# Kernel optimization log

Measured on AMD Instinct MI355X. Metric: run time of the kernel, lower is better.

## Reference

```python
import jax, jax.numpy as jnp
import numpy as np

PI = float(np.pi)


def _make_grid(H, W, stride, k, delta):
    """Gnomonic (tangent-plane) sampling grid for one spherical conv layer.
    Returns rows (Ho, K) and cols (Ho, Wo, K) of fractional pixel coords."""
    Ho, Wo = H // stride, W // stride
    j = jnp.arange(k, dtype=jnp.float32) - (k - 1) / 2.0
    t = jnp.tan(delta / k * j)                      # tangent-plane tap coords
    yy = jnp.repeat(t, k)                           # (K,) vertical
    xx = jnp.tile(t, k)                             # (K,) horizontal
    rho = jnp.sqrt(xx ** 2 + yy ** 2)
    rho_s = jnp.where(rho == 0, 1.0, rho)
    nu = jnp.arctan(rho)
    # latitude of each output row center (equirect: row -> colatitude)
    lat0 = PI / 2 - (jnp.arange(Ho, dtype=jnp.float32) * stride + 0.5) * (PI / H)
    sl, cl = jnp.sin(lat0)[:, None], jnp.cos(lat0)[:, None]   # (Ho,1)
    sn, cn = jnp.sin(nu)[None, :], jnp.cos(nu)[None, :]       # (1,K)
    lat = jnp.arcsin(jnp.clip(cn * sl + (yy[None, :] / rho_s[None, :]) * sn * cl, -1.0, 1.0))
    dlon = jnp.arctan2(xx[None, :] * sn, rho[None, :] * cl * cn - yy[None, :] * sl * sn)
    rows = (PI / 2 - lat) / PI * H - 0.5            # (Ho,K) fractional row
    dcol = dlon / (2 * PI) * W                      # (Ho,K) longitude offset in px
    cols = (jnp.arange(Wo, dtype=jnp.float32) * stride)[None, :, None] + dcol[:, None, :]
    return rows, cols


def _bilinear(x, rows, cols):
    """x: (B,C,H,W); rows (Ho,K); cols (Ho,Wo,K). Latitude clamped, longitude wrapped.
    Returns patches (B,C,Ho,Wo,K)."""
    B, C, H, W = x.shape
    r0 = jnp.floor(rows); wr = (rows - r0)[:, None, :]
    c0 = jnp.floor(cols); wc = cols - c0
    r0i = jnp.clip(r0, 0, H - 1).astype(jnp.int32)
    r1i = jnp.clip(r0 + 1, 0, H - 1).astype(jnp.int32)
    c0i = jnp.mod(c0.astype(jnp.int32), W)
    c1i = jnp.mod(c0i + 1, W)

    def g(ri, ci):
        return x[:, :, ri[:, None, :], ci]          # (B,C,Ho,Wo,K)

    return (g(r0i, c0i) * (1 - wr) * (1 - wc) + g(r0i, c1i) * (1 - wr) * wc
            + g(r1i, c0i) * wr * (1 - wc) + g(r1i, c1i) * wr * wc)


def _sconv(x, w, b, delta, stride):
    k = int(round(np.sqrt(w.shape[-1])))
    rows, cols = _make_grid(x.shape[2], x.shape[3], stride, k, delta)
    p = _bilinear(x, rows, cols)                    # (B,C,Ho,Wo,K)
    return jnp.einsum('bchwk,ock->bohw', p, w) + b[None, :, None, None]


def _bn_relu(x, g, b):
    m = x.mean((0, 2, 3), keepdims=True)
    v = jnp.mean((x - m) ** 2, (0, 2, 3), keepdims=True)  # biased var (torch BN train)
    return jax.nn.relu((x - m) / jnp.sqrt(v + 1e-5) * g[None, :, None, None] + b[None, :, None, None])


def _up2(x):
    return jnp.repeat(jnp.repeat(x, 2, axis=2), 2, axis=3)


def _forward(input, w1, b1, g1, bb1, w2, b2, g2, bb2, w3, b3, g3, bb3,
             w31, b31, g31, bb31, w4, b4, g4, bb4, w41, b41, g41, bb41,
             w5, b5, g5, bb5, w6, b6, g6, bb6):
    x1 = _bn_relu(_sconv(input, w1, b1, PI / 32, 2), g1, bb1)
    x2 = _bn_relu(_sconv(x1, w2, b2, PI / 16, 2), g2, bb2)
    x3 = _bn_relu(_sconv(x2, w3, b3, PI / 4, 2), g3, bb3)
    x31 = _bn_relu(_sconv(x3, w31, b31, PI / 4, 1), g31, bb31)
    x4 = _bn_relu(_sconv(x31, w4, b4, PI / 2, 2), g4, bb4)
    x41 = _bn_relu(_sconv(x4, w41, b41, PI / 2, 1), g41, bb41)
    x5 = _bn_relu(_sconv(jnp.concatenate([_up2(x41), x31], 1), w5, b5, PI / 4, 1), g5, bb5)
    x6 = _bn_relu(_sconv(jnp.concatenate([_up2(x5), x2], 1), w6, b6, PI / 8, 1), g6, bb6)
    return x6


_CFGS = [('1', 32, 6, 7), ('2', 64, 32, 5), ('3', 128, 64, 5), ('31', 128, 128, 3),
         ('4', 256, 128, 3), ('41', 256, 256, 3), ('5', 256, 384, 3), ('6', 128, 320, 3)]


def setup_inputs() -> dict:
    key = jax.random.key(0)
    inp = {'input': jax.random.normal(jax.random.fold_in(key, 0), (4, 6, 256, 512), jnp.float32)}
    for i, (s, o, c, kk) in enumerate(_CFGS):
        kw = jax.random.fold_in(key, i + 1)
        inp['w' + s] = jax.random.normal(kw, (o, c, kk * kk), jnp.float32) / np.float32(np.sqrt(c * kk * kk))
        inp['b' + s] = jnp.zeros((o,), jnp.float32)
        inp['g' + s] = jnp.ones((o,), jnp.float32)
        inp['bb' + s] = jnp.zeros((o,), jnp.float32)
    return inp


def reference(input, w1, b1, g1, bb1, w2, b2, g2, bb2, w3, b3, g3, bb3,
              w31, b31, g31, bb31, w4, b4, g4, bb4, w41, b41, g41, bb41,
              w5, b5, g5, bb5, w6, b6, g6, bb6):
    return _forward(input, w1, b1, g1, bb1, w2, b2, g2, bb2, w3, b3, g3, bb3,
                    w31, b31, g31, bb31, w4, b4, g4, bb4, w41, b41, g41, bb41,
                    w5, b5, g5, bb5, w6, b6, g6, bb6)
```

## Files before the change

### kernel.cpp

```cpp
#include <hip/hip_runtime.h>
#include <cstddef>
#include <cstdint>

#define PI_F 3.14159265358979323846f

typedef __attribute__((ext_vector_type(8))) short short8;
typedef __attribute__((ext_vector_type(4))) float floatx4;

template<int V> struct IC { static constexpr int value = V; };

__device__ __forceinline__ short f2bf(float f) {
    union { float f; unsigned u; } v; v.f = f;
    unsigned r = v.u + 0x7FFFu + ((v.u >> 16) & 1u);
    return (short)(r >> 16);
}

__global__ __launch_bounds__(256) void wtrans_kernel(
    const float* __restrict__ A, short* __restrict__ Abf,
    int M, int Mpad, int K2, int C, int Cp, int Kp, int Korig)
{
    int idx = blockIdx.x * 256 + threadIdx.x;
    if (idx >= Mpad * Kp) return;
    int m = idx / Kp;
    int k = idx - m * Kp;
    int tap = (unsigned)k / (unsigned)Cp;
    int c   = k - tap * Cp;
    float v = 0.f;
    if (m < M && tap < K2 && c < C) v = A[(size_t)m * Korig + c * K2 + tap];
    Abf[idx] = f2bf(v);
}

__global__ __launch_bounds__(256) void zero_kernel(float* __restrict__ p, int n)
{
    int i = blockIdx.x * 256 + threadIdx.x;
    if (i < n) p[i] = 0.f;
}

__global__ __launch_bounds__(256) void zero3_kernel(
    float* __restrict__ a, int na, float* __restrict__ b, int nb,
    float* __restrict__ c, int nc)
{
    int i = blockIdx.x * 256 + threadIdx.x;
    if (i < na) { a[i] = 0.f; return; }
    i -= na;
    if (i < nb) { b[i] = 0.f; return; }
    i -= nb;
    if (i < nc) c[i] = 0.f;
}

#define BNT 64
#define BKT 32
#define LDK 40

template<int MW, int SK, int LGW, int UP, int LGWO, int CS>
__global__ __launch_bounds__(256) void sconv_mfma_kernel(
    const short* __restrict__ Abf,
    const float* __restrict__ src1, const float* __restrict__ src2,
    float2* __restrict__ part, int nBlkN,
    int C1, int Ctot, int Cp, int H, int W, int up1,
    int K2, int ksz, int stride, int lWo, int lHo, float delta,
    float* __restrict__ Y, int M, int Kp, int N, int lgM)
{
    __shared__ short Bs[(LGW != 0) ? 1 : 2][BNT][LDK];
    __shared__ float4 tab[64];
    extern __shared__ __align__(16) char dynLds[];

    constexpr int LGSK = (SK == 1) ? 0 : ((SK == 2) ? 1 : 2);

    const int tid = threadIdx.x;
    const int total = gridDim.x;
    const int pid = blockIdx.x;
    const int logical = (pid & 7) * (total >> 3) + (pid >> 3);
    const int mblk = logical & ((1 << lgM) - 1);
    const int rest = logical >> lgM;
    const int kslice = rest & (SK - 1);
    const int nblk = rest >> LGSK;
    const int m0 = mblk * (MW * 64);
    const int n0 = nblk * BNT;

    const int Wo  = 1 << lWo;
    const int Ho  = 1 << lHo;
    const int HW  = 1 << (lWo + lHo);

    const int nHo  = (lWo >= 6) ? 1 : (BNT >> lWo);
    const int nEnt = nHo * K2;
    const int hoBase = (n0 >> lWo) & (Ho - 1);
    if (tid < nEnt) {
        int hoL = tid / K2;
        int i   = tid - hoL * K2;
        int ho_g = hoBase + hoL;
        int jy = i / ksz, jx = i - jy * ksz;
        float halfk = (ksz - 1) * 0.5f;
        float yy = tanf(delta / (float)ksz * ((float)jy - halfk));
        float xx = tanf(delta / (float)ksz * ((float)jx - halfk));
        float rho = sqrtf(xx * xx + yy * yy);
        float rho_s = (rho == 0.f) ? 1.f : rho;
        float nu = atanf(rho);
        float lat0 = PI_F * 0.5f - ((float)(ho_g * stride) + 0.5f) * (PI_F / (float)H);
        float sl = sinf(lat0), cl = cosf(lat0);
        float sn = sinf(nu),  cn = cosf(nu);
        float arg = cn * sl + (yy / rho_s) * sn * cl;
        arg = fminf(1.f, fmaxf(-1.f, arg));
        float lat = asinf(arg);
        float dlon = atan2f(xx * sn, rho * cl * cn - yy * sl * sn);
        float row = (PI_F * 0.5f - lat) / PI_F * (float)H - 0.5f;
        float dcol = dlon / (2.f * PI_F) * (float)W;
        float r0f = floorf(row);
        float fr = row - r0f;
        int r0 = (int)r0f;
        int r0i = min(max(r0, 0), H - 1);
        int r1i = min(max(r0 + 1, 0), H - 1);
        tab[tid] = make_float4(fr, dcol, __int_as_float(r0i), __int_as_float(r1i));
    }

    const int nn    = tid & 63;
    const int kslot = tid >> 6;
    const int n_s  = n0 + nn;
    const int wo_s = n_s & (Wo - 1);
    const int hoL_s = nn >> lWo;
    const int b_s  = n_s >> (lWo + lHo);
    const int tabBase = hoL_s * K2;
    const float wo_px = (float)(wo_s * stride);
    const int Hs = H >> up1, Ws = W >> up1;
    const int plane1 = Hs * Ws;
    const int plane2 = H * W;
    const unsigned boff1 = (unsigned)__builtin_amdgcn_readfirstlane(
        (int)(b_s * C1 * plane1));
    const unsigned boff2 = (unsigned)__builtin_amdgcn_readfirstlane(
        (int)(b_s * (Ctot - C1) * plane2));

    const int Tper = (Kp / BKT) / SK;
    const int t0 = kslice * Tper;
    const bool smallC = (Cp < 32);
    int tap, cb;
    if (smallC) { tap = kslot; cb = 0; }
    else {
        int prog = t0 * BKT;
        tap = prog / Cp;
        cb  = prog - tap * Cp + kslot * 8;
    }
    const int dtap = smallC ? (32 / Cp) : 0;

    const int wave = tid >> 6;
    const int wrow = wave * (MW * 16);
    const int lane = tid & 63;
    const int l16  = lane & 15;
    const int quad = lane >> 4;

    const short* pA[MW];
#pragma unroll
    for (int i = 0; i < MW; i++)
        pA[i] = Abf + (size_t)(m0 + wrow + i * 16 + l16) * Kp + quad * 8;

    floatx4 acc[MW][4];
#pragma unroll
    for (int i = 0; i < MW; i++)
#pragma unroll
        for (int j = 0; j < 4; j++)
            acc[i][j] = (floatx4){0.f, 0.f, 0.f, 0.f};

    if constexpr (LGW == 0) {
        __syncthreads();

        for (int t = t0; t < t0 + Tper; t++) {
            const int k0 = t * BKT;
            const int buf = t & 1;
            const int tapS = __builtin_amdgcn_readfirstlane(tap);
            const int cbS  = __builtin_amdgcn_readfirstlane(cb);
            {
                const int tapc = min(tapS, K2 - 1);
                const float4 e = tab[tabBase + tapc];
                const float fr = e.x;
                const float col = wo_px + e.y;
                const int r0i = __float_as_int(e.z);
                const int r1i = __float_as_int(e.w);
                const float cf = floorf(col);
                const float fc = col - cf;
                const int c0 = ((int)cf) & (W - 1);
                const int c1 = (c0 + 1) & (W - 1);
                const float w11 = fr * fc;
                const float w10 = fr - w11;
                const float w01 = fc - w11;
                const float w00 = 1.f - fr - fc + w11;

                const char* sbase; unsigned o00, o01, o10, o11, planeB;
                if (cbS < C1) {
                    const int ra = (r0i >> up1) * Ws, rb = (r1i >> up1) * Ws;
                    const int ca = c0 >> up1, cx = c1 >> up1;
                    const unsigned base = boff1 + (unsigned)cbS * (unsigned)plane1;
                    o00 = (base + ra + ca) * 4u; o01 = (base + ra + cx) * 4u;
                    o10 = (base + rb + ca) * 4u; o11 = (base + rb + cx) * 4u;
                    planeB = (unsigned)plane1 * 4u; sbase = (const char*)src1;
                } else {
                    const int ra = r0i * W, rb = r1i * W;
                    const unsigned base = boff2 + (unsigned)(cbS - C1) * (unsigned)plane2;
                    o00 = (base + ra + c0) * 4u; o01 = (base + ra + c1) * 4u;
                    o10 = (base + rb + c0) * 4u; o11 = (base + rb + c1) * 4u;
                    planeB = (unsigned)plane2 * 4u; sbase = (const char*)src2;
                }

                if constexpr (CS > 0) {
                    float q00[CS], q01[CS], q10[CS], q11[CS];
#pragma unroll
                    for (int j = 0; j < CS; j++) {
                        q00[j] = *(const float*)(sbase + o00);
                        q01[j] = *(const float*)(sbase + o01);
                        q10[j] = *(const float*)(sbase + o10);
                        q11[j] = *(const float*)(sbase + o11);
                        o00 += planeB; o01 += planeB; o10 += planeB; o11 += planeB;
                    }
                    unsigned pk[4];
#pragma unroll
                    for (int jj = 0; jj < 4; jj++) {
                        if (2 * jj < CS) {
                            float v0 = w00 * q00[2 * jj] + w01 * q01[2 * jj]
                                     + w10 * q10[2 * jj] + w11 * q11[2 * jj];
                            float v1 = 0.f;
                            if (2 * jj + 1 < CS)
                                v1 = w00 * q00[2 * jj + 1] + w01 * q01[2 * jj + 1]
                                   + w10 * q10[2 * jj + 1] + w11 * q11[2 * jj + 1];
                            unsigned rr;
                            asm("v_cvt_pk_bf16_f32 %0, %1, %2"
                                : "=v"(rr) : "v"(v0), "v"(v1));
                            pk[jj] = rr;
                        } else {
                            pk[jj] = 0u;
                        }
                    }
                    *(uint4*)&Bs[buf][nn][kslot * 8] =
                        make_uint4(pk[0], pk[1], pk[2], pk[3]);
                } else {
                    float q00[8], q01[8], q10[8], q11[8];
#pragma unroll
                    for (int j = 0; j < 8; j++) {
                        q00[j] = *(const float*)(sbase + o00);
                        q01[j] = *(const float*)(sbase + o01);
                        q10[j] = *(const float*)(sbase + o10);
                        q11[j] = *(const float*)(sbase + o11);
                        o00 += planeB; o01 += planeB; o10 += planeB; o11 += planeB;
                    }
                    unsigned pk[4];
#pragma unroll
                    for (int jj = 0; jj < 4; jj++) {
                        float v0 = w00 * q00[2 * jj]     + w01 * q01[2 * jj]
                                 + w10 * q10[2 * jj]     + w11 * q11[2 * jj];
                        float v1 = w00 * q00[2 * jj + 1] + w01 * q01[2 * jj + 1]
                                 + w10 * q10[2 * jj + 1] + w11 * q11[2 * jj + 1];
                        unsigned r;
                        asm("v_cvt_pk_bf16_f32 %0, %1, %2"
                            : "=v"(r) : "v"(v0), "v"(v1));
                        pk[jj] = r;
                    }
                    *(uint4*)&Bs[buf][nn][kslot * 8] =
                        make_uint4(pk[0], pk[1], pk[2], pk[3]);
                }
            }
            __syncthreads();

            short8 af[MW];
#pragma unroll
            for (int i = 0; i < MW; i++)
                af[i] = *(const short8*)(pA[i] + k0);
            short8 bfv[4];
#pragma unroll
            for (int j = 0; j < 4; j++)
                bfv[j] = *(const short8*)&Bs[buf][j * 16 + l16][quad * 8];
#pragma unroll
            for (int i = 0; i < MW; i++)
#pragma unroll
                for (int j = 0; j < 4; j++)
                    acc[i][j] = __builtin_amdgcn_mfma_f32_16x16x32_bf16(
                        af[i], bfv[j], acc[i][j], 0, 0, 0);

            if (smallC) { tap += dtap; }
            else { cb += 32; if (cb >= Cp) { cb -= Cp; tap++; } }
        }
    } else {
        constexpr int WC    = 1 << LGW;
        constexpr int LGWS1 = LGW - UP;
        constexpr int NHO   = (LGWO >= 6) ? 1 : (64 >> LGWO);
        constexpr int NHO2  = NHO * 2;
        constexpr int LG2NHO = (NHO == 4) ? 3 : ((NHO == 2) ? 2 : 1);
        constexpr int NU    = 64 * NHO;
        const int kslotU = __builtin_amdgcn_readfirstlane(kslot);

        auto stageTile = [&](int tapT, int cbT) {
            const bool s1 = (cbT < C1);
            const float* srcT = s1 ? src1 : src2;
            const int lgWt = s1 ? LGWS1 : LGW;
            const int upT  = s1 ? UP : 0;
            const int plT  = s1 ? plane1 : plane2;
            const unsigned chB = s1
                ? (boff1 + (unsigned)cbT * (unsigned)plane1)
                : (boff2 + (unsigned)(cbT - C1) * (unsigned)plane2);
            const int tapc2 = min(tapT, K2 - 1);
            const int lgLPU = lgWt - 2;
            const int NIw = (NU << lgWt) >> 10;
            const int uW  = lane >> lgLPU;
            const unsigned colB = (unsigned)(lane & ((1 << lgLPU) - 1)) << 2;
            for (int ii = 0; ii < NIw; ii++) {
                const int idx = kslotU * NIw + ii;
                const int u = (idx << (6 - lgLPU)) + uW;
                const int chL = u >> LG2NHO;
                const int rem = u & (NHO2 - 1);
                const int hoL = rem & (NHO - 1);
                const float4 e = tab[hoL * K2 + tapc2];
                const float rsel = (rem >> (LG2NHO - 1)) ? e.w : e.z;
                const int r = __float_as_int(rsel) >> upT;
                const float* gp = srcT + (chB + (unsigned)chL * (unsigned)plT
                                          + ((unsigned)r << lgWt) + colB);
                __builtin_amdgcn_global_load_lds(
                    (const __attribute__((address_space(1))) void*)gp,
                    (__attribute__((address_space(3))) void*)(dynLds + (size_t)idx * 1024),
                    16, 0, 0);
            }
        };

        int tapS, cb0S;
        {
            int prog = t0 * BKT;
            tapS = prog / Cp;
            cb0S = prog - tapS * Cp;
        }

        __syncthreads();

        stageTile(tapS, cb0S);
        short8 afc[MW];
#pragma unroll
        for (int i2 = 0; i2 < MW; i2++)
            afc[i2] = *(const short8*)(pA[i2] + t0 * BKT);

        for (int t = t0; t < t0 + Tper; t++) {
            tapS = __builtin_amdgcn_readfirstlane(tapS);
            cb0S = __builtin_amdgcn_readfirstlane(cb0S);
            const bool isS1 = (cb0S < C1);
            const int tapcI  = min(tapS, K2 - 1);

            asm volatile("s_waitcnt vmcnt(0)" ::: "memory");
            __syncthreads();

            auto interpStore = [&](auto lgwc, auto upc) {
                constexpr int LGWSRC = decltype(lgwc)::value;
                constexpr int UPX    = decltype(upc)::value;
                constexpr int STEPR  = NHO << LGWSRC;
                constexpr int STEPC  = NHO2 << LGWSRC;
                const float4 e2 = tab[tabBase + tapcI];
                const float fr = e2.x;
                const float col = wo_px + e2.y;
                const float cf = floorf(col);
                const float fc = col - cf;
                const int c0 = ((int)cf) & (WC - 1);
                const int c1 = (c0 + 1) & (WC - 1);
                const int c0s = c0 >> UPX, c1s = c1 >> UPX;
                const float w11 = fr * fc;
                const float w10 = fr - w11;
                const float w01 = fc - w11;
                const float w00 = 1.f - fr - fc + w11;
                const float* rowsF = (const float*)dynLds;
                const float* pc0 = rowsF
                    + ((((kslot * 8) << LG2NHO) + hoL_s) << LGWSRC) + c0s;
                const float* pc1 = pc0 + (c1s - c0s);
                float vv[8];
#pragma unroll
                for (int j = 0; j < 8; j++) {
                    const float x00 = pc0[0];
                    const float x10 = pc0[STEPR];
                    const float x01 = pc1[0];
                    const float x11 = pc1[STEPR];
                    vv[j] = w00 * x00 + w01 * x01 + w10 * x10 + w11 * x11;
                    pc0 += STEPC; pc1 += STEPC;
                }
                unsigned pk[4];
#pragma unroll
                for (int jj = 0; jj < 4; jj++) {
                    unsigned rr;
                    asm("v_cvt_pk_bf16_f32 %0, %1, %2"
                        : "=v"(rr) : "v"(vv[2 * jj]), "v"(vv[2 * jj + 1]));
                    pk[jj] = rr;
                }
                *(uint4*)&Bs[0][nn][kslot * 8] =
                    make_uint4(pk[0], pk[1], pk[2], pk[3]);
            };
            if (isS1) interpStore(IC<LGWS1>{}, IC<UP>{});
            else      interpStore(IC<LGW>{},   IC<0>{});

            __syncthreads();

            int tapN = tapS, cbN = cb0S + BKT;
            if (cbN >= Cp) { cbN = 0; tapN = tapS + 1; }
            const bool more = (t + 1 < t0 + Tper);
            short8 afn[MW];
            if (more) {
#pragma unroll
                for (int i2 = 0; i2 < MW; i2++)
                    afn[i2] = *(const short8*)(pA[i2] + (t + 1) * BKT);
                stageTile(tapN, cbN);
            }

            short8 bfr[4];
#pragma unroll
            for (int j = 0; j < 4; j++)
                bfr[j] = *(const short8*)&Bs[0][j * 16 + l16][quad * 8];
#pragma unroll
            for (int i2 = 0; i2 < MW; i2++)
#pragma unroll
                for (int j = 0; j < 4; j++)
                    acc[i2][j] = __builtin_amdgcn_mfma_f32_16x16x32_bf16(
                        afc[i2], bfr[j], acc[i2][j], 0, 0, 0);

            tapS = tapN; cb0S = cbN;
            if (more) {
#pragma unroll
                for (int i2 = 0; i2 < MW; i2++) afc[i2] = afn[i2];
            }
        }
    }

    if (SK == 1) {
#pragma unroll
        for (int i = 0; i < MW; i++) {
#pragma unroll
            for (int rr = 0; rr < 4; rr++) {
                const int m = m0 + wrow + i * 16 + quad * 4 + rr;
                const bool mv = (m < M);
                float s = 0.f, q = 0.f;
#pragma unroll
                for (int j = 0; j < 4; j++) {
                    const int n = n0 + j * 16 + l16;
                    const float v = acc[i][j][rr];
                    s += v; q += v * v;
                    if (mv) {
                        const int wo = n & (Wo - 1);
                        const int r  = n >> lWo;
                        const int ho = r & (Ho - 1);
                        const int b_ = r >> lHo;
                        Y[((size_t)b_ * M + m) * HW + (ho << lWo) + wo] = v;
                    }
                }
#pragma unroll
                for (int mask = 1; mask < 16; mask <<= 1) {
                    s += __shfl_xor(s, mask);
                    q += __shfl_xor(q, mask);
                }
                if (mv && l16 == 0)
                    part[(size_t)m * nBlkN + nblk] = make_float2(s, q);
            }
        }
    } else {
#pragma unroll
        for (int i = 0; i < MW; i++) {
#pragma unroll
            for (int j = 0; j < 4; j++) {
                const int n = n0 + j * 16 + l16;
                const int wo = n & (Wo - 1);
                const int r  = n >> lWo;
                const int ho = r & (Ho - 1);
                const int b_ = r >> lHo;
#pragma unroll
                for (int rr = 0; rr < 4; rr++) {
                    const int m = m0 + wrow + i * 16 + quad * 4 + rr;
                    if (m < M)
                        unsafeAtomicAdd(
                            &Y[((size_t)b_ * M + m) * HW + (ho << lWo) + wo],
                            acc[i][j][rr]);
                }
            }
        }
    }
}

__global__ __launch_bounds__(256) void bn_stats8_kernel(
    const float* __restrict__ Y, float2* __restrict__ part,
    int Co, int HW, int B)
{
    int co = blockIdx.x;
    int sp = blockIdx.y;
    int tid = threadIdx.x;
    int Nt = B * HW;
    int len = Nt >> 3;
    int start = sp * len, end = start + len;
    float s = 0.f, q = 0.f;
    for (int idx = start + tid; idx < end; idx += 256) {
        int b = idx / HW; int o = idx - b * HW;
        float v = Y[((size_t)b * Co + co) * HW + o];
        s += v; q += v * v;
    }
    __shared__ float sh_s[256], sh_q[256];
    sh_s[tid] = s; sh_q[tid] = q;
    __syncthreads();
    for (int off = 128; off > 0; off >>= 1) {
        if (tid < off) { sh_s[tid] += sh_s[tid + off]; sh_q[tid] += sh_q[tid + off]; }
        __syncthreads();
    }
    if (tid == 0)
        part[co * 8 + sp] = make_float2(sh_s[0], sh_q[0]);
}

__global__ __launch_bounds__(256) void bn_finalize_kernel(
    const float2* __restrict__ part, float2* __restrict__ scSf,
    const float* __restrict__ g, const float* __restrict__ bb,
    int nBlkN, int Nt)
{
    int c = blockIdx.x;
    int tid = threadIdx.x;
    double s = 0.0, q = 0.0;
    for (int k = tid; k < nBlkN; k += 256) {
        float2 p = part[(size_t)c * nBlkN + k];
        s += p.x; q += p.y;
    }
    __shared__ double sh_s[256], sh_q[256];
    sh_s[tid] = s; sh_q[tid] = q;
    __syncthreads();
    for (int off = 128; off > 0; off >>= 1) {
        if (tid < off) { sh_s[tid] += sh_s[tid + off]; sh_q[tid] += sh_q[tid + off]; }
        __syncthreads();
    }
    if (tid == 0) {
        double mean = sh_s[0] / Nt;
        double var = sh_q[0] / Nt - mean * mean;
        if (var < 0.0) var = 0.0;
        float sc = g[c] / sqrtf((float)var + 1e-5f);
        scSf[c] = make_float2(sc, bb[c] - (float)mean * sc);
    }
}

__global__ __launch_bounds__(256) void bn_apply_kernel(
    float* __restrict__ Y, const float2* __restrict__ scSf,
    int Co, int HW, int total)
{
    int idx = blockIdx.x * 256 + threadIdx.x;
    if (idx >= total) return;
    int c = (idx / HW) % Co;
    float2 s = scSf[c];
    float v = Y[idx] * s.x + s.y;
    Y[idx] = v > 0.f ? v : 0.f;
}

__global__ __launch_bounds__(256) void bn_apply_sk_kernel(
    float* __restrict__ Y, const float2* __restrict__ part,
    const float* __restrict__ g, const float* __restrict__ bb,
    int Co, int HW, int Nt, int total)
{
    int idx = blockIdx.x * 256 + threadIdx.x;
    int c = (idx / HW) % Co;
    __shared__ float s_sc, s_sf;
    if (threadIdx.x == 0) {
        double s = 0.0, q = 0.0;
        for (int p = 0; p < 8; p++) {
            float2 pp = part[c * 8 + p];
            s += pp.x; q += pp.y;
        }
        double mean = s / Nt;
        double var = q / Nt - mean * mean;
        if (var < 0.0) var = 0.0;
        float sc = g[c] / sqrtf((float)var + 1e-5f);
        s_sc = sc;
        s_sf = bb[c] - (float)mean * sc;
    }
    __syncthreads();
    if (idx >= total) return;
    float v = Y[idx] * s_sc + s_sf;
    Y[idx] = v > 0.f ? v : 0.f;
}

extern "C" void kernel_launch(void* const* d_in, const int* in_sizes, int n_in,
                              void* d_out, int out_size, void* d_ws, size_t ws_size,
                              hipStream_t stream)
{
    const int B = 4;
    char* ws = (char*)d_ws;
    size_t off = 0;
    auto allocb = [&](size_t bytes) -> void* {
        void* p = ws + off;
        off = (off + bytes + 255) & ~(size_t)255;
        return p;
    };

    float2* part = (float2*)allocb((size_t)65536 * sizeof(float2));
    float2* scSf = (float2*)allocb(256 * sizeof(float2));
    float* x2  = (float*)allocb((size_t)B * 64  * 64 * 128 * 4);
    float* x31 = (float*)allocb((size_t)B * 128 * 32 * 64 * 4);
    float* Q   = (float*)allocb((size_t)B * 32  * 128 * 256 * 4);
    float* x1  = Q;
    float* x3  = Q;
    float* x4  = Q;
    float* x41 = Q + (size_t)B * 256 * 16 * 32;
    float* x5  = Q + 2 * (size_t)B * 256 * 16 * 32;

    static const int kH[8]  = {256, 128,  64,  32,  32,  16,  32,  64};
    static const int kW[8]  = {512, 256, 128,  64,  64,  32,  64, 128};
    static const int kK[8]  = {  7,   5,   5,   3,   3,   3,   3,   3};
    static const int kSt[8] = {  2,   2,   2,   1,   2,   1,   1,   1};
    static const int kC[8]  = {  6,  32,  64, 128, 128, 256, 384, 320};
    static const int kM[8]  = { 32,  64, 128, 128, 256, 256, 256, 128};
    static const int kMW[8] = {  1,   1,   1,   1,   1,   1,   2,   2};
    static const int kSK[8] = {  1,   2,   4,   4,   4,   4,   4,   2};

    int Cp_[8], Kp_[8], Mpad_[8];
    short* Abf[8];
    for (int i = 0; i < 8; i++) {
        int K2 = kK[i] * kK[i];
        int Cp = (kC[i] < 8) ? 8 : kC[i];
        int gran = 32 * kSK[i];
        int Kp = (K2 * Cp + gran - 1) / gran * gran;
        int Mpad = (kM[i] + 63) & ~63;
        Cp_[i] = Cp; Kp_[i] = Kp; Mpad_[i] = Mpad;
        Abf[i] = (short*)allocb((size_t)Mpad * Kp * sizeof(short));
    }
    (void)ws_size; (void)in_sizes; (void)n_in; (void)out_size;

    struct LCfg { const float *s1, *s2; int C1, up; float delta; int widx; float* Y; };
    const float* input = (const float*)d_in[0];
    LCfg L[8] = {
        { input, nullptr,   6, 0, PI_F / 32.f,  1, x1  },
        { x1,    nullptr,  32, 0, PI_F / 16.f,  5, x2  },
        { x2,    nullptr,  64, 0, PI_F / 4.f,   9, x3  },
        { x3,    nullptr, 128, 0, PI_F / 4.f,  13, x31 },
        { x31,   nullptr, 128, 0, PI_F / 2.f,  17, x4  },
        { x4,    nullptr, 256, 0, PI_F / 2.f,  21, x41 },
        { x41,   x31,     256, 1, PI_F / 4.f,  25, x5  },
        { x5,    x2,      256, 1, PI_F / 8.f,  29, (float*)d_out },
    };

    {
        int n_x2 = B * 64 * 64 * 128;
        int n_x31 = B * 128 * 32 * 64;
        int n_out = B * 128 * 64 * 128;
        int tot = n_x2 + n_x31 + n_out;
        zero3_kernel<<<dim3((tot + 255) / 256), dim3(256), 0, stream>>>(
            x2, n_x2, x31, n_x31, (float*)d_out, n_out);
    }

    for (int i = 0; i < 8; i++) {
        const LCfg& c = L[i];
        int H = kH[i], W = kW[i], k = kK[i], st = kSt[i];
        int Ho = H / st, Wo = W / st;
        int K2 = k * k;
        int C  = kC[i], M = kM[i];
        int HW = Ho * Wo;
        int N  = B * HW;
        int lWo = __builtin_ctz(Wo), lHo = __builtin_ctz(Ho);
        const float* Wt   = (const float*)d_in[c.widx];
        const float* gam  = (const float*)d_in[c.widx + 2];
        const float* bet  = (const float*)d_in[c.widx + 3];
        int total = B * M * HW;

        int tn = Mpad_[i] * Kp_[i];
        wtrans_kernel<<<dim3((tn + 255) / 256), dim3(256), 0, stream>>>(
            Wt, Abf[i], M, Mpad_[i], K2, C, Cp_[i], Kp_[i], C * K2);

        int MWi = kMW[i], SKi = kSK[i];
        int nBlkM = Mpad_[i] / (64 * MWi);
        int nBlkN = N / BNT;
        int totalBlk = nBlkN * nBlkM * SKi;
        int lgM = __builtin_ctz(nBlkM);

        size_t dynB = 0;
        if (i >= 2) {
            int nHo_i = (Wo >= 64) ? 1 : (64 / Wo);
            int w1 = W >> c.up;
            int wmax = c.s2 ? W : w1;
            if (w1 > wmax) wmax = w1;
            dynB = (size_t)(64 * nHo_i) * (size_t)wmax * 4u;
        }

        if (SKi > 1 && i >= 2 && i <= 6 && c.Y != x31)
            zero_kernel<<<dim3((total + 255) / 256), dim3(256), 0, stream>>>(
                c.Y, total);

        #define CONV_ARGS Abf[i], c.s1, c.s2, part, nBlkN, \
            c.C1, C, Cp_[i], H, W, c.up, K2, k, st, lWo, lHo, c.delta, \
            c.Y, M, Kp_[i], N, lgM
        #define LAUNCH(MW_, SK_, LGW_, UP_, LGWO_, CS_, DYN_) \
            sconv_mfma_kernel<MW_,SK_,LGW_,UP_,LGWO_,CS_> \
                <<<dim3(totalBlk), dim3(256), DYN_, stream>>>(CONV_ARGS)
        switch (i) {
            case 0: LAUNCH(1, 1, 0, 0, 0, 6, 0);    break;
            case 1: LAUNCH(1, 2, 0, 0, 0, 0, 0);    break;
            case 2: LAUNCH(1, 4, 7, 0, 6, 0, dynB); break;
            case 3: LAUNCH(1, 4, 6, 0, 6, 0, dynB); break;
            case 4: LAUNCH(1, 4, 6, 0, 5, 0, dynB); break;
            case 5: LAUNCH(1, 4, 5, 0, 5, 0, dynB); break;
            case 6: LAUNCH(2, 4, 6, 1, 6, 0, dynB); break;
            case 7: LAUNCH(2, 2, 7, 1, 7, 0, dynB); break;
        }
        #undef LAUNCH
        #undef CONV_ARGS

        if (SKi > 1) {
            bn_stats8_kernel<<<dim3(M, 8), dim3(256), 0, stream>>>(
                c.Y, part, M, HW, B);
            bn_apply_sk_kernel<<<dim3(total / 256), dim3(256), 0, stream>>>(
                c.Y, part, gam, bet, M, HW, N, total);
        } else {
            bn_finalize_kernel<<<dim3(M), dim3(256), 0, stream>>>(
                part, scSf, gam, bet, nBlkN, N);
            bn_apply_kernel<<<dim3(total / 256), dim3(256), 0, stream>>>(
                c.Y, scSf, M, HW, total);
        }
    }
}
```

Before: 694.7 us.

## Software-pipeline bilinear gather loads one K-step ahead in LGW==0 path

Restructures the LGW==0 main loop so the four-corner global gathers for the next K tile are issued before interpolating, storing and running MFMAs on the current tile, using two ping-pong register sets. This aims to hide gather latency behind the bf16 conversion, LDS store and MFMA work. The cost is extra VGPRs for a second set of gathered values, which may lower occupancy. Issuing one step ahead also makes the last iteration read one extra tap, which the existing min clamp on tap keeps in bounds.

```diff
diff --git a/kernel.cpp b/kernel.cpp
--- a/kernel.cpp
+++ b/kernel.cpp
@@ -160,103 +160,85 @@
             acc[i][j] = (floatx4){0.f, 0.f, 0.f, 0.f};
 
     if constexpr (LGW == 0) {
-        __syncthreads();
-
-        for (int t = t0; t < t0 + Tper; t++) {
+        constexpr int CSX = (CS > 0) ? CS : 8;
+        struct QS {
+            float q00[CSX], q01[CSX], q10[CSX], q11[CSX];
+            float w00, w01, w10, w11;
+        };
+        QS qa, qb;
+
+        auto issueQ = [&](QS& q) {
+            const int tapS = __builtin_amdgcn_readfirstlane(tap);
+            const int cbS  = __builtin_amdgcn_readfirstlane(cb);
+            const int tapc = min(tapS, K2 - 1);
+            const float4 e = tab[tabBase + tapc];
+            const float fr = e.x;
+            const float col = wo_px + e.y;
+            const int r0i = __float_as_int(e.z);
+            const int r1i = __float_as_int(e.w);
+            const float cf = floorf(col);
+            const float fc = col - cf;
+            const int c0 = ((int)cf) & (W - 1);
+            const int c1 = (c0 + 1) & (W - 1);
+            const float w11 = fr * fc;
+            q.w11 = w11;
+            q.w10 = fr - w11;
+            q.w01 = fc - w11;
+            q.w00 = 1.f - fr - fc + w11;
+
+            const char* sbase; unsigned o00, o01, o10, o11, planeB;
+            if (cbS < C1) {
+                const int ra = (r0i >> up1) * Ws, rb = (r1i >> up1) * Ws;
+                const int ca = c0 >> up1, cx = c1 >> up1;
+                const unsigned base = boff1 + (unsigned)cbS * (unsigned)plane1;
+                o00 = (base + ra + ca) * 4u; o01 = (base + ra + cx) * 4u;
+                o10 = (base + rb + ca) * 4u; o11 = (base + rb + cx) * 4u;
+                planeB = (unsigned)plane1 * 4u; sbase = (const char*)src1;
+            } else {
+                const int ra = r0i * W, rb = r1i * W;
+                const unsigned base = boff2 + (unsigned)(cbS - C1) * (unsigned)plane2;
+                o00 = (base + ra + c0) * 4u; o01 = (base + ra + c1) * 4u;
+                o10 = (base + rb + c0) * 4u; o11 = (base + rb + c1) * 4u;
+                planeB = (unsigned)plane2 * 4u; sbase = (const char*)src2;
+            }
+#pragma unroll
+            for (int j = 0; j < CSX; j++) {
+                q.q00[j] = *(const float*)(sbase + o00);
+                q.q01[j] = *(const float*)(sbase + o01);
+                q.q10[j] = *(const float*)(sbase + o10);
+                q.q11[j] = *(const float*)(sbase + o11);
+                o00 += planeB; o01 += planeB; o10 += planeB; o11 += planeB;
+            }
+            if (smallC) { tap += dtap; }
+            else { cb += 32; if (cb >= Cp) { cb -= Cp; tap++; } }
+        };
+
+        auto interpStoreD = [&](const QS& q, int buf) {
+            unsigned pk[4];
+#pragma unroll
+            for (int jj = 0; jj < 4; jj++) {
+                if (2 * jj < CSX) {
+                    float v0 = q.w00 * q.q00[2 * jj] + q.w01 * q.q01[2 * jj]
+                             + q.w10 * q.q10[2 * jj] + q.w11 * q.q11[2 * jj];
+                    float v1 = 0.f;
+                    if (2 * jj + 1 < CSX)
+                        v1 = q.w00 * q.q00[2 * jj + 1] + q.w01 * q.q01[2 * jj + 1]
+                           + q.w10 * q.q10[2 * jj + 1] + q.w11 * q.q11[2 * jj + 1];
+                    unsigned rr;
+                    asm("v_cvt_pk_bf16_f32 %0, %1, %2"
+                        : "=v"(rr) : "v"(v0), "v"(v1));
+                    pk[jj] = rr;
+                } else {
+                    pk[jj] = 0u;
+                }
+            }
+            *(uint4*)&Bs[buf][nn][kslot * 8] =
+                make_uint4(pk[0], pk[1], pk[2], pk[3]);
+        };
+
+        auto mfmaStep = [&](int t) {
             const int k0 = t * BKT;
             const int buf = t & 1;
-            const int tapS = __builtin_amdgcn_readfirstlane(tap);
-            const int cbS  = __builtin_amdgcn_readfirstlane(cb);
-            {
-                const int tapc = min(tapS, K2 - 1);
-                const float4 e = tab[tabBase + tapc];
-                const float fr = e.x;
-                const float col = wo_px + e.y;
-                const int r0i = __float_as_int(e.z);
-                const int r1i = __float_as_int(e.w);
-                const float cf = floorf(col);
-                const float fc = col - cf;
-                const int c0 = ((int)cf) & (W - 1);
-                const int c1 = (c0 + 1) & (W - 1);
-                const float w11 = fr * fc;
-                const float w10 = fr - w11;
-                const float w01 = fc - w11;
-                const float w00 = 1.f - fr - fc + w11;
-
-                const char* sbase; unsigned o00, o01, o10, o11, planeB;
-                if (cbS < C1) {
-                    const int ra = (r0i >> up1) * Ws, rb = (r1i >> up1) * Ws;
-                    const int ca = c0 >> up1, cx = c1 >> up1;
-                    const unsigned base = boff1 + (unsigned)cbS * (unsigned)plane1;
-                    o00 = (base + ra + ca) * 4u; o01 = (base + ra + cx) * 4u;
-                    o10 = (base + rb + ca) * 4u; o11 = (base + rb + cx) * 4u;
-                    planeB = (unsigned)plane1 * 4u; sbase = (const char*)src1;
-                } else {
-                    const int ra = r0i * W, rb = r1i * W;
-                    const unsigned base = boff2 + (unsigned)(cbS - C1) * (unsigned)plane2;
-                    o00 = (base + ra + c0) * 4u; o01 = (base + ra + c1) * 4u;
-                    o10 = (base + rb + c0) * 4u; o11 = (base + rb + c1) * 4u;
-                    planeB = (unsigned)plane2 * 4u; sbase = (const char*)src2;
-                }
-
-                if constexpr (CS > 0) {
-                    float q00[CS], q01[CS], q10[CS], q11[CS];
-#pragma unroll
-                    for (int j = 0; j < CS; j++) {
-                        q00[j] = *(const float*)(sbase + o00);
-                        q01[j] = *(const float*)(sbase + o01);
-                        q10[j] = *(const float*)(sbase + o10);
-                        q11[j] = *(const float*)(sbase + o11);
-                        o00 += planeB; o01 += planeB; o10 += planeB; o11 += planeB;
-                    }
-                    unsigned pk[4];
-#pragma unroll
-                    for (int jj = 0; jj < 4; jj++) {
-                        if (2 * jj < CS) {
-                            float v0 = w00 * q00[2 * jj] + w01 * q01[2 * jj]
-                                     + w10 * q10[2 * jj] + w11 * q11[2 * jj];
-                            float v1 = 0.f;
-                            if (2 * jj + 1 < CS)
-                                v1 = w00 * q00[2 * jj + 1] + w01 * q01[2 * jj + 1]
-                                   + w10 * q10[2 * jj + 1] + w11 * q11[2 * jj + 1];
-                            unsigned rr;
-                            asm("v_cvt_pk_bf16_f32 %0, %1, %2"
-                                : "=v"(rr) : "v"(v0), "v"(v1));
-                            pk[jj] = rr;
-                        } else {
-                            pk[jj] = 0u;
-                        }
-                    }
-                    *(uint4*)&Bs[buf][nn][kslot * 8] =
-                        make_uint4(pk[0], pk[1], pk[2], pk[3]);
-                } else {
-                    float q00[8], q01[8], q10[8], q11[8];
-#pragma unroll
-                    for (int j = 0; j < 8; j++) {
-                        q00[j] = *(const float*)(sbase + o00);
-                        q01[j] = *(const float*)(sbase + o01);
-                        q10[j] = *(const float*)(sbase + o10);
-                        q11[j] = *(const float*)(sbase + o11);
-                        o00 += planeB; o01 += planeB; o10 += planeB; o11 += planeB;
-                    }
-                    unsigned pk[4];
-#pragma unroll
-                    for (int jj = 0; jj < 4; jj++) {
-                        float v0 = w00 * q00[2 * jj]     + w01 * q01[2 * jj]
-                                 + w10 * q10[2 * jj]     + w11 * q11[2 * jj];
-                        float v1 = w00 * q00[2 * jj + 1] + w01 * q01[2 * jj + 1]
-                                 + w10 * q10[2 * jj + 1] + w11 * q11[2 * jj + 1];
-                        unsigned r;
-                        asm("v_cvt_pk_bf16_f32 %0, %1, %2"
-                            : "=v"(r) : "v"(v0), "v"(v1));
-                        pk[jj] = r;
-                    }
-                    *(uint4*)&Bs[buf][nn][kslot * 8] =
-                        make_uint4(pk[0], pk[1], pk[2], pk[3]);
-                }
-            }
-            __syncthreads();
-
             short8 af[MW];
 #pragma unroll
             for (int i = 0; i < MW; i++)
@@ -271,9 +253,26 @@
                 for (int j = 0; j < 4; j++)
                     acc[i][j] = __builtin_amdgcn_mfma_f32_16x16x32_bf16(
                         af[i], bfv[j], acc[i][j], 0, 0, 0);
-
-            if (smallC) { tap += dtap; }
-            else { cb += 32; if (cb >= Cp) { cb -= Cp; tap++; } }
+        };
+
+        __syncthreads();
+
+        issueQ(qa);
+        int t = t0;
+        for (; t + 2 <= t0 + Tper; t += 2) {
+            issueQ(qb);
+            interpStoreD(qa, t & 1);
+            __syncthreads();
+            mfmaStep(t);
+            issueQ(qa);
+            interpStoreD(qb, (t + 1) & 1);
+            __syncthreads();
+            mfmaStep(t + 1);
+        }
+        if (t < t0 + Tper) {
+            interpStoreD(qa, t & 1);
+            __syncthreads();
+            mfmaStep(t);
         }
     } else {
         constexpr int WC    = 1 << LGW;
```

Result: no change. 683.8 us (-1.6%).
